# Kernel tuning notes

Hardware: AMD Instinct MI355X
Metric: run time of the kernel (lower is better)

The kernel has to match this reference:

```python
import jax, jax.numpy as jnp
import numpy as np

B, S, D, H, HD = 1, 2048, 1024, 16, 64
GH = 64            # GammaGate hidden dim
FFN_H = int(D * 4 * 2 / 3)
CTX = 512          # omega-rule context window c
LAM = 0.999        # base exponential decay

def _rms(x, w, eps=1e-6):
    return x * jax.lax.rsqrt(jnp.mean(x * x, axis=-1, keepdims=True) + eps) * w

def _rope(q, k):
    hd = q.shape[-1]; s = q.shape[2]
    inv = 1.0 / (10000.0 ** (jnp.arange(0, hd, 2, dtype=jnp.float32) / hd))
    fr = jnp.arange(s, dtype=jnp.float32)[:, None] * inv[None, :]
    cos = jnp.concatenate([jnp.cos(fr), jnp.cos(fr)], -1)
    sin = jnp.concatenate([jnp.sin(fr), jnp.sin(fr)], -1)
    rot = lambda x: jnp.concatenate([-x[..., hd // 2:], x[..., :hd // 2]], -1)
    return q * cos + rot(q) * sin, k * cos + rot(k) * sin

def setup_inputs() -> dict:
    key = jax.random.key(0)
    ks = jax.random.split(key, 10)
    n = lambda i, sh, s=0.02: jax.random.normal(ks[i], sh, jnp.float32) * s
    return dict(
        x=jax.random.normal(ks[0], (B, S, D), jnp.float32),
        norm1_w=jnp.ones((D,), jnp.float32),
        norm2_w=jnp.ones((D,), jnp.float32),
        w_qkv=n(1, (D, 3 * D)),
        q_norm_w=jnp.ones((HD,), jnp.float32),
        k_norm_w=jnp.ones((HD,), jnp.float32),
        gamma_w1=n(2, (D, GH)),
        gamma_w2=n(3, (GH, 1)),
        m_persist=n(4, (H, HD, HD)),
        memory_gate=jnp.array([-3.0], jnp.float32),
        w_o=n(5, (D, D), 0.02 / 2 ** 0.5),
        ffn_w1=n(6, (D, FFN_H)),
        ffn_w3=n(7, (D, FFN_H)),
        ffn_w2=n(8, (FFN_H, D)),
    )

def reference(x, norm1_w, norm2_w, w_qkv, q_norm_w, k_norm_w, gamma_w1, gamma_w2,
              m_persist, memory_gate, w_o, ffn_w1, ffn_w3, ffn_w2):
    b, s, d = x.shape
    h = _rms(x, norm1_w)
    qkv = h @ w_qkv
    q, k, v = jnp.split(qkv, 3, axis=-1)
    rs = lambda t: t.reshape(b, s, H, HD).transpose(0, 2, 1, 3)   # (b,h,s,hd)
    q, k, v = rs(q), rs(k), rs(v)
    q = _rms(q, q_norm_w); k = _rms(k, k_norm_w)                  # qk_norm
    q, k = _rope(q, k)
    # input-dependent gamma gate: Linear->SiLU->Linear->Sigmoid
    gamma = jax.nn.sigmoid(jax.nn.silu(h @ gamma_w1) @ gamma_w2)  # (b,s,1)
    # Omega-rule memory: Q'_t = (M_p q_t + sum_i w_{t,i} k_i (k_i . q_t)) / (1 + sum_i w_{t,i})
    ti = jnp.arange(s)
    delta = ti[:, None] - ti[None, :]
    wmask = (delta >= 0) & (delta < CTX)
    decay = jnp.where(wmask, LAM ** delta.astype(jnp.float32), 0.0)      # (t,i)
    w = decay[None, None] * gamma[:, None, None, :, 0]                   # (b,1,t,i)
    norm = 1.0 + jnp.sum(w, axis=-1)                                     # (b,1,t)
    scores = jnp.einsum('bhtd,bhid->bhti', q, k)
    contrib = jnp.einsum('bhti,bhid->bhtd', w * scores, k)
    persist = jnp.einsum('hde,bhte->bhtd', m_persist, q)
    qp = (persist + contrib) / norm[..., None]
    gate = jax.nn.sigmoid(memory_gate)[0]
    q = (1.0 - gate) * q + gate * qp
    # causal attention
    aw = jnp.einsum('bhtd,bhid->bhti', q, k) * (HD ** -0.5)
    causal = ti[:, None] >= ti[None, :]
    aw = jnp.where(causal[None, None], aw, -jnp.inf)
    aw = jax.nn.softmax(aw, axis=-1)
    ao = jnp.einsum('bhti,bhid->bhtd', aw, v).transpose(0, 2, 1, 3).reshape(b, s, d)
    x = x + ao @ w_o
    h2 = _rms(x, norm2_w)
    x = x + (jax.nn.silu(h2 @ ffn_w1) * (h2 @ ffn_w3)) @ ffn_w2   # SwiGLU
    return x
```

## Files before the change

### kernel.cpp

```cpp
#include <hip/hip_runtime.h>
#include <hip/hip_bf16.h>

#define S_LEN 2048
#define D_DIM 1024
#define H_NUM 16
#define HD_DIM 64
#define GH_DIM 64
#define FFN_H 2730
#define FFNP  2816
#define CTX_W 512
#define L2LAM -0.00144341687f
#define QBLK 64
#define KBLK 64
#define ALDK 76
#define QSCALE 0.1803368801111731f

typedef unsigned short u16;
typedef __attribute__((ext_vector_type(8))) short bf16x8_t;
typedef __attribute__((ext_vector_type(4))) float f32x4_t;

__device__ inline float wave_sum(float v) {
    for (int off = 32; off; off >>= 1) v += __shfl_xor(v, off);
    return v;
}
__device__ inline u16 f2bf(float f) {
    unsigned r;
    asm("v_cvt_pk_bf16_f32 %0, %1, %2" : "=v"(r) : "v"(f), "v"(f));
    return (u16)r;
}
__device__ inline unsigned f2bf2(float lo, float hi) {
    unsigned r;
    asm("v_cvt_pk_bf16_f32 %0, %1, %2" : "=v"(r) : "v"(lo), "v"(hi));
    return r;
}
__device__ inline float bf2f(u16 u) {
    return __uint_as_float(((unsigned int)u) << 16);
}
__device__ inline void gload16(const void* g, void* l) {
    __builtin_amdgcn_global_load_lds(
        (const __attribute__((address_space(1))) void*)g,
        (__attribute__((address_space(3))) void*)l, 16, 0, 0);
}

template<bool GAMMA>
__global__ __launch_bounds__(256) void rmsnorm_gamma_kernel(
    const float* __restrict__ in, const float* __restrict__ w,
    u16* __restrict__ out, const float* __restrict__ w1,
    const float* __restrict__ w2, float* __restrict__ gamma)
{
    __shared__ float hl[D_DIM];
    __shared__ float part[4][GH_DIM];
    __shared__ float wsum[4];
    int row = blockIdx.x;
    int tid = threadIdx.x, lane = tid & 63, wv = tid >> 6;
    const float4* ir = reinterpret_cast<const float4*>(in + (size_t)row * D_DIM);
    float4 v = ir[tid];
    float ss = v.x*v.x + v.y*v.y + v.z*v.z + v.w*v.w;
    ss = wave_sum(ss);
    if (lane == 0) wsum[wv] = ss;
    __syncthreads();
    float tot = wsum[0] + wsum[1] + wsum[2] + wsum[3];
    float scale = rsqrtf(tot / (float)D_DIM + 1e-6f);
    const float4* wr = reinterpret_cast<const float4*>(w);
    float4 wv4 = wr[tid];
    float h0 = v.x * scale * wv4.x, h1 = v.y * scale * wv4.y;
    float h2 = v.z * scale * wv4.z, h3 = v.w * scale * wv4.w;
    uint2 o;
    o.x = f2bf2(h0, h1);
    o.y = f2bf2(h2, h3);
    *reinterpret_cast<uint2*>(out + (size_t)row * D_DIM + tid * 4) = o;
    if (GAMMA) {
        hl[tid*4+0] = h0; hl[tid*4+1] = h1; hl[tid*4+2] = h2; hl[tid*4+3] = h3;
        __syncthreads();
        float acc = 0.f;
        #pragma unroll 8
        for (int k = wv * 256; k < wv * 256 + 256; ++k)
            acc += hl[k] * w1[k * GH_DIM + lane];
        part[wv][lane] = acc;
        __syncthreads();
        if (wv == 0) {
            float t = part[0][lane] + part[1][lane] + part[2][lane] + part[3][lane];
            float z = t / (1.f + __expf(-t));
            float y = z * w2[lane];
            float t2 = wave_sum(y);
            if (lane == 0) gamma[row] = 1.f / (1.f + __expf(-t2));
        }
    }
}

__global__ __launch_bounds__(256) void prep_kernel(
    const float* __restrict__ w_qkv, const float* __restrict__ w_o,
    const float* __restrict__ w1f, const float* __restrict__ w3f,
    const float* __restrict__ w2f, u16* __restrict__ wqT,
    u16* __restrict__ woT, u16* __restrict__ w13T, u16* __restrict__ w2T,
    const float* __restrict__ x, const float* __restrict__ norm1_w,
    u16* __restrict__ h_bf, const float* __restrict__ gw1,
    const float* __restrict__ gw2, float* __restrict__ gamma)
{
    __shared__ float tile[64][65];
    __shared__ float part[4][GH_DIM];
    __shared__ float wsum[4];
    int b = blockIdx.x;
    int tid = threadIdx.x;
    if (b < 3136) {
        const float* src; u16* dst;
        int srcK, srcN, Kp, rowOff, rowMul, nbx;
        if (b < 768)       {           src = w_qkv; dst = wqT;  srcK = 1024; srcN = 3072; Kp = 1024; rowOff = 0; rowMul = 1; nbx = 48; }
        else if (b < 1024) { b -= 768;  src = w_o;  dst = woT;  srcK = 1024; srcN = 1024; Kp = 1024; rowOff = 0; rowMul = 1; nbx = 16; }
        else if (b < 1728) { b -= 1024; src = w1f;  dst = w13T; srcK = 1024; srcN = 2730; Kp = 1024; rowOff = 0; rowMul = 2; nbx = 44; }
        else if (b < 2432) { b -= 1728; src = w3f;  dst = w13T; srcK = 1024; srcN = 2730; Kp = 1024; rowOff = 1; rowMul = 2; nbx = 44; }
        else               { b -= 2432; src = w2f;  dst = w2T;  srcK = 2730; srcN = 1024; Kp = 2816; rowOff = 0; rowMul = 1; nbx = 16; }
        int n0 = (b % nbx) * 64, k0 = (b / nbx) * 64;
        int tx = tid & 15, ty = tid >> 4;
        bool interior = (k0 + 63 < srcK) && (n0 + 63 < srcN);
        #pragma unroll
        for (int p = 0; p < 4; ++p) {
            int kk = p * 16 + ty;
            int r = k0 + kk;
            int cb = n0 + tx * 4;
            float4 v;
            if (interior) {
                v = *(const float4*)(src + (size_t)r * srcN + cb);
            } else {
                v.x = (r < srcK && cb     < srcN) ? src[(size_t)r * srcN + cb]     : 0.f;
                v.y = (r < srcK && cb + 1 < srcN) ? src[(size_t)r * srcN + cb + 1] : 0.f;
                v.z = (r < srcK && cb + 2 < srcN) ? src[(size_t)r * srcN + cb + 2] : 0.f;
                v.w = (r < srcK && cb + 3 < srcN) ? src[(size_t)r * srcN + cb + 3] : 0.f;
            }
            tile[kk][tx*4+0] = v.x; tile[kk][tx*4+1] = v.y;
            tile[kk][tx*4+2] = v.z; tile[kk][tx*4+3] = v.w;
        }
        __syncthreads();
        int wx = tid & 7, wy = tid >> 3;
        #pragma unroll
        for (int p = 0; p < 2; ++p) {
            int nn = p * 32 + wy;
            int ks = wx * 8;
            uint4 o;
            o.x = f2bf2(tile[ks+0][nn], tile[ks+1][nn]);
            o.y = f2bf2(tile[ks+2][nn], tile[ks+3][nn]);
            o.z = f2bf2(tile[ks+4][nn], tile[ks+5][nn]);
            o.w = f2bf2(tile[ks+6][nn], tile[ks+7][nn]);
            *(uint4*)(dst + (size_t)(rowOff + (size_t)(n0 + nn) * rowMul) * Kp + k0 + ks) = o;
        }
    } else {
        int row = b - 3136;
        int lane = tid & 63, wv = tid >> 6;
        float* hl = &tile[0][0];
        const float4* ir = reinterpret_cast<const float4*>(x + (size_t)row * D_DIM);
        float4 v = ir[tid];
        float ss = v.x*v.x + v.y*v.y + v.z*v.z + v.w*v.w;
        ss = wave_sum(ss);
        if (lane == 0) wsum[wv] = ss;
        __syncthreads();
        float tot = wsum[0] + wsum[1] + wsum[2] + wsum[3];
        float scale = rsqrtf(tot / (float)D_DIM + 1e-6f);
        const float4* wr = reinterpret_cast<const float4*>(norm1_w);
        float4 wv4 = wr[tid];
        float h0 = v.x * scale * wv4.x, h1 = v.y * scale * wv4.y;
        float h2 = v.z * scale * wv4.z, h3 = v.w * scale * wv4.w;
        uint2 o;
        o.x = f2bf2(h0, h1);
        o.y = f2bf2(h2, h3);
        *reinterpret_cast<uint2*>(h_bf + (size_t)row * D_DIM + tid * 4) = o;
        hl[tid*4+0] = h0; hl[tid*4+1] = h1; hl[tid*4+2] = h2; hl[tid*4+3] = h3;
        __syncthreads();
        float acc = 0.f;
        #pragma unroll 8
        for (int k = wv * 256; k < wv * 256 + 256; ++k)
            acc += hl[k] * gw1[k * GH_DIM + lane];
        part[wv][lane] = acc;
        __syncthreads();
        if (wv == 0) {
            float t = part[0][lane] + part[1][lane] + part[2][lane] + part[3][lane];
            float z = t / (1.f + __expf(-t));
            float y = z * gw2[lane];
            float t2 = wave_sum(y);
            if (lane == 0) gamma[row] = 1.f / (1.f + __expf(-t2));
        }
    }
}

__global__ __launch_bounds__(256) void split_rope_tr_kernel(
    const u16* __restrict__ qkv, const float* __restrict__ qw,
    const float* __restrict__ kw, float* __restrict__ qhp,
    u16* __restrict__ khp, u16* __restrict__ khT, u16* __restrict__ vhT)
{
    __shared__ u16 tk[64][ALDK];
    __shared__ u16 tv[64][ALDK];
    int tid = threadIdx.x;
    int w = tid >> 6, d = tid & 63;
    int h = blockIdx.y;
    int s0 = blockIdx.x * 64;
    float qwv = qw[d], kwv = kw[d];
    int j = d & 31;
    float inv = expf(-(float)j * (9.2103403719761836f / 32.0f));
    float sgn = (d < 32) ? -1.f : 1.f;
    for (int i = 0; i < 16; ++i) {
        int sl = w * 16 + i;
        int s = s0 + sl;
        size_t base = (size_t)s * (3 * D_DIM) + h * HD_DIM + d;
        float qv = bf2f(qkv[base]);
        float kv = bf2f(qkv[base + D_DIM]);
        u16  vv = qkv[base + 2 * D_DIM];
        float sq = wave_sum(qv * qv);
        float qn = qv * rsqrtf(sq / (float)HD_DIM + 1e-6f) * qwv;
        float sk = wave_sum(kv * kv);
        float kn = kv * rsqrtf(sk / (float)HD_DIM + 1e-6f) * kwv;
        float ang = (float)s * inv;
        float cs = cosf(ang), sn = sinf(ang);
        float qp = __shfl_xor(qn, 32);
        float kp = __shfl_xor(kn, 32);
        float qo = qn * cs + sgn * qp * sn;
        float ko = kn * cs + sgn * kp * sn;
        size_t ob = ((size_t)h * S_LEN + s) * HD_DIM + d;
        u16 kb = f2bf(ko);
        qhp[ob] = qo;
        khp[ob] = kb;
        tk[sl][d] = kb;
        tv[sl][d] = vv;
    }
    __syncthreads();
    int r = tid >> 2, cc = (tid & 3) * 16;
    union { u16 u[16]; bf16x8_t v[2]; } ok, ov;
    #pragma unroll
    for (int e = 0; e < 16; ++e) {
        int ksrc = (e & 3) * 16 + (tid & 3) * 4 + (e >> 2);
        ok.u[e] = tk[ksrc][r]; ov.u[e] = tv[ksrc][r];
    }
    u16* kd = khT + ((size_t)h * HD_DIM + r) * S_LEN + s0 + cc;
    u16* vd = vhT + ((size_t)h * HD_DIM + r) * S_LEN + s0 + cc;
    *(bf16x8_t*)kd       = ok.v[0];
    *(bf16x8_t*)(kd + 8) = ok.v[1];
    *(bf16x8_t*)vd       = ov.v[0];
    *(bf16x8_t*)(vd + 8) = ov.v[1];
}

template<int BM, int MODE>
__global__ __launch_bounds__(256) void gemm_bb_kernel(
    const u16* __restrict__ A, const u16* __restrict__ B,
    u16* __restrict__ Cb, int M, int N, int K)
{
    constexpr int MREP = BM / 32;
    constexpr int ACH  = BM / 32;
    __shared__ u16 As[BM * 64];
    __shared__ u16 Bs[128 * 64];
    int tid = threadIdx.x, lane = tid & 63, wid = tid >> 6;
    int wr = wid >> 1, wc = wid & 1;
    int row0 = blockIdx.y * BM, col0 = blockIdx.x * 128;
    int l8 = lane >> 3, l7 = lane & 7;
    f32x4_t acc[MREP][4];
    #pragma unroll
    for (int i = 0; i < MREP; ++i)
        #pragma unroll
        for (int j = 0; j < 4; ++j) acc[i][j] = (f32x4_t)0.f;

    int fr = lane & 15, fo = (lane >> 4) * 8;
    for (int k0 = 0; k0 < K; k0 += 64) {
        #pragma unroll
        for (int i = 0; i < ACH; ++i) {
            int ch = wid * ACH + i;
            const u16* ga = A + (size_t)(row0 + ch * 8 + l8) * K + k0 + l7 * 8;
            gload16(ga, &As[ch * 512]);
        }
        #pragma unroll
        for (int i = 0; i < 4; ++i) {
            int ch = wid * 4 + i;
            const u16* gb = B + (size_t)(col0 + ch * 8 + l8) * K + k0 + l7 * 8;
            gload16(gb, &Bs[ch * 512]);
        }
        __syncthreads();
        __builtin_amdgcn_s_setprio(1);
        #pragma unroll
        for (int khf = 0; khf < 2; ++khf) {
            bf16x8_t bfrag[4];
            #pragma unroll
            for (int ni = 0; ni < 4; ++ni)
                bfrag[ni] = *(const bf16x8_t*)&Bs[(wc * 64 + ni * 16 + fr) * 64 + khf * 32 + fo];
            #pragma unroll
            for (int mi = 0; mi < MREP; ++mi) {
                bf16x8_t af = *(const bf16x8_t*)&As[(wr * (BM / 2) + mi * 16 + fr) * 64 + khf * 32 + fo];
                #pragma unroll
                for (int ni = 0; ni < 4; ++ni)
                    acc[mi][ni] = __builtin_amdgcn_mfma_f32_16x16x32_bf16(
                        af, bfrag[ni], acc[mi][ni], 0, 0, 0);
            }
        }
        __builtin_amdgcn_s_setprio(0);
        __syncthreads();
    }
    int dr = (lane >> 4) * 4, dc = lane & 15;
    #pragma unroll
    for (int mi = 0; mi < MREP; ++mi) {
        int gr = row0 + wr * (BM / 2) + mi * 16 + dr;
        #pragma unroll
        for (int ni = 0; ni < 4; ++ni) {
            int gc = col0 + wc * 64 + ni * 16 + dc;
            #pragma unroll
            for (int j = 0; j < 4; ++j) {
                float v = acc[mi][ni][j];
                if (MODE == 1) {
                    Cb[(size_t)(gr + j) * N + gc] = f2bf(v);
                } else {
                    float partner = __shfl_xor(v, 1);
                    float a1 = (dc & 1) ? partner : v;
                    float a3 = (dc & 1) ? v : partner;
                    float rr = a1 / (1.f + __expf(-a1)) * a3;
                    if (!(dc & 1))
                        Cb[(size_t)(gr + j) * (N >> 1) + (gc >> 1)] = f2bf(rr);
                }
            }
        }
    }
}

__global__ __launch_bounds__(256) void gemm64_kernel(
    const u16* __restrict__ A, const u16* __restrict__ B,
    const float* __restrict__ res, float* __restrict__ Cf,
    int M, int N, int K)
{
    __shared__ u16 As[64 * 64];
    __shared__ u16 Bs[64 * 64];
    int tid = threadIdx.x, lane = tid & 63, wid = tid >> 6;
    int wr = wid >> 1, wc = wid & 1;
    int row0 = blockIdx.y * 64, col0 = blockIdx.x * 64;
    int l8 = lane >> 3, l7 = lane & 7;
    f32x4_t acc[2][2];
    #pragma unroll
    for (int i = 0; i < 2; ++i)
        #pragma unroll
        for (int j = 0; j < 2; ++j) acc[i][j] = (f32x4_t)0.f;
    int fr = lane & 15, fo = (lane >> 4) * 8;
    for (int k0 = 0; k0 < K; k0 += 64) {
        #pragma unroll
        for (int i = 0; i < 2; ++i) {
            int ch = wid * 2 + i;
            const u16* ga = A + (size_t)(row0 + ch * 8 + l8) * K + k0 + l7 * 8;
            gload16(ga, &As[ch * 512]);
            const u16* gb = B + (size_t)(col0 + ch * 8 + l8) * K + k0 + l7 * 8;
            gload16(gb, &Bs[ch * 512]);
        }
        __syncthreads();
        __builtin_amdgcn_s_setprio(1);
        #pragma unroll
        for (int khf = 0; khf < 2; ++khf) {
            bf16x8_t bfrag[2];
            #pragma unroll
            for (int ni = 0; ni < 2; ++ni)
                bfrag[ni] = *(const bf16x8_t*)&Bs[(wc * 32 + ni * 16 + fr) * 64 + khf * 32 + fo];
            #pragma unroll
            for (int mi = 0; mi < 2; ++mi) {
                bf16x8_t af = *(const bf16x8_t*)&As[(wr * 32 + mi * 16 + fr) * 64 + khf * 32 + fo];
                #pragma unroll
                for (int ni = 0; ni < 2; ++ni)
                    acc[mi][ni] = __builtin_amdgcn_mfma_f32_16x16x32_bf16(
                        af, bfrag[ni], acc[mi][ni], 0, 0, 0);
            }
        }
        __builtin_amdgcn_s_setprio(0);
        __syncthreads();
    }
    int dr = (lane >> 4) * 4, dc = lane & 15;
    #pragma unroll
    for (int mi = 0; mi < 2; ++mi) {
        int gr = row0 + wr * 32 + mi * 16 + dr;
        #pragma unroll
        for (int ni = 0; ni < 2; ++ni) {
            int gc = col0 + wc * 32 + ni * 16 + dc;
            #pragma unroll
            for (int j = 0; j < 4; ++j) {
                size_t off = (size_t)(gr + j) * N + gc;
                Cf[off] = acc[mi][ni][j] + res[off];
            }
        }
    }
}

__global__ __launch_bounds__(256) void fused_omega_attn_kernel(
    const float* __restrict__ qhp, const u16* __restrict__ khp,
    const u16* __restrict__ khT, const u16* __restrict__ vhT,
    const float* __restrict__ gammab, const float* __restrict__ mp,
    const float* __restrict__ mg, u16* __restrict__ ao)
{
    __shared__ u16 Ks[2][KBLK][ALDK];
    __shared__ u16 Xt[2][KBLK][ALDK];
    __shared__ u16 Ps[QBLK][ALDK];
    __shared__ float colfL[CTX_W + KBLK];
    const int tid = threadIdx.x, lane = tid & 63, wq = tid >> 6;
    const int b = blockIdx.x;
    const int hi = (b >> 8) & 1;
    const int h = ((b & 7) << 1) + hi;
    const int s5 = (b >> 3) & 31;
    const int qt = hi ? (31 - s5) : s5;
    const int q0 = qt * QBLK;
    const int fr = lane & 15, g4 = lane >> 4;
    const int fko = g4 * 8;
    const int c = fr, rg = g4;
    const int si = tid >> 2, sdb = (tid & 3) * 16;
    const size_t hS = (size_t)h * S_LEN;
    const size_t hD = (size_t)h * HD_DIM;

    int rowt[4]; float rowf[4];
    #pragma unroll
    for (int j = 0; j < 4; ++j) {
        rowt[j] = q0 + wq * 16 + rg * 4 + j;
        rowf[j] = exp2f((float)(wq * 16 + rg * 4 + j) * L2LAM);
    }
    bf16x8_t qf[2];
    {
        const float* qrow = qhp + (hS + q0 + wq * 16 + fr) * HD_DIM;
        #pragma unroll
        for (int u = 0; u < 2; ++u) {
            float4 a = *(const float4*)(qrow + u * 32 + fko);
            float4 bq = *(const float4*)(qrow + u * 32 + fko + 4);
            bf16x8_t f;
            f[0]=f2bf(a.x); f[1]=f2bf(a.y); f[2]=f2bf(a.z); f[3]=f2bf(a.w);
            f[4]=f2bf(bq.x); f[5]=f2bf(bq.y); f[6]=f2bf(bq.z); f[7]=f2bf(bq.w);
            qf[u] = f;
        }
    }
    f32x4_t accc[4];
    #pragma unroll
    for (int n = 0; n < 4; ++n) accc[n] = (f32x4_t)0.f;
    float wsum[4] = {0.f, 0.f, 0.f, 0.f};
    const int kt0 = (q0 > (CTX_W - 1)) ? (q0 - (CTX_W - 1)) / KBLK : 0;
    const int i0 = kt0 * KBLK;
    const int nwin = (qt + 1) * KBLK - i0;
    for (int idx = tid; idx < nwin; idx += 256) {
        int icol = i0 + idx;
        colfL[idx] = exp2f((float)(q0 - icol) * L2LAM) * gammab[icol];
    }
    {
        const u16* gk = khp + (hS + kt0 * KBLK + si) * HD_DIM + sdb;
        const u16* gx = khT + (hD + si) * S_LEN + kt0 * KBLK + sdb;
        *(bf16x8_t*)&Ks[0][si][sdb]     = *(const bf16x8_t*)gk;
        *(bf16x8_t*)&Ks[0][si][sdb + 8] = *(const bf16x8_t*)(gk + 8);
        *(bf16x8_t*)&Xt[0][si][sdb]     = *(const bf16x8_t*)gx;
        *(bf16x8_t*)&Xt[0][si][sdb + 8] = *(const bf16x8_t*)(gx + 8);
    }
    __syncthreads();
    int cur = 0;
    for (int kt = kt0; kt <= qt; ++kt) {
        const int k0 = kt * KBLK;
        const bool hn = (kt < qt);
        bf16x8_t nk0, nk1, nx0, nx1;
        if (hn) {
            const u16* gk = khp + (hS + k0 + KBLK + si) * HD_DIM + sdb;
            const u16* gx = khT + (hD + si) * S_LEN + k0 + KBLK + sdb;
            nk0 = *(const bf16x8_t*)gk; nk1 = *(const bf16x8_t*)(gk + 8);
            nx0 = *(const bf16x8_t*)gx; nx1 = *(const bf16x8_t*)(gx + 8);
        }
        f32x4_t s[4];
        #pragma unroll
        for (int n = 0; n < 4; ++n) s[n] = (f32x4_t)0.f;
        __builtin_amdgcn_s_setprio(1);
        #pragma unroll
        for (int u = 0; u < 2; ++u)
            #pragma unroll
            for (int n = 0; n < 4; ++n) {
                bf16x8_t kb = *(const bf16x8_t*)&Ks[cur][n * 16 + fr][u * 32 + fko];
                s[n] = __builtin_amdgcn_mfma_f32_16x16x32_bf16(qf[u], kb, s[n], 0, 0, 0);
            }
        __builtin_amdgcn_s_setprio(0);
        const bool boundary = (kt == kt0) || (kt == qt);
        float colf[4];
        #pragma unroll
        for (int n = 0; n < 4; ++n)
            colf[n] = colfL[k0 - i0 + n * 16 + c];
        #pragma unroll
        for (int j = 0; j < 4; ++j) {
            float pv[4];
            #pragma unroll
            for (int n = 0; n < 4; ++n) {
                float w;
                if (boundary) {
                    int delta = rowt[j] - (k0 + n * 16 + c);
                    w = (delta >= 0 && delta < CTX_W) ? rowf[j] * colf[n] : 0.f;
                } else {
                    w = rowf[j] * colf[n];
                }
                wsum[j] += w;
                pv[n] = w * s[n][j];
            }
            uint2 pk;
            pk.x = f2bf2(pv[0], pv[1]);
            pk.y = f2bf2(pv[2], pv[3]);
            *(uint2*)&Ps[wq * 16 + rg * 4 + j][c * 4] = pk;
        }
        __builtin_amdgcn_s_setprio(1);
        #pragma unroll
        for (int u = 0; u < 2; ++u) {
            bf16x8_t pa = *(const bf16x8_t*)&Ps[wq * 16 + fr][u * 32 + fko];
            #pragma unroll
            for (int n = 0; n < 4; ++n) {
                bf16x8_t kb = *(const bf16x8_t*)&Xt[cur][n * 16 + fr][u * 32 + fko];
                accc[n] = __builtin_amdgcn_mfma_f32_16x16x32_bf16(pa, kb, accc[n], 0, 0, 0);
            }
        }
        __builtin_amdgcn_s_setprio(0);
        if (hn) {
            int nxt = cur ^ 1;
            *(bf16x8_t*)&Ks[nxt][si][sdb]     = nk0;
            *(bf16x8_t*)&Ks[nxt][si][sdb + 8] = nk1;
            *(bf16x8_t*)&Xt[nxt][si][sdb]     = nx0;
            *(bf16x8_t*)&Xt[nxt][si][sdb + 8] = nx1;
        }
        __syncthreads();
        cur ^= 1;
    }
    f32x4_t pacc[4];
    #pragma unroll
    for (int n = 0; n < 4; ++n) pacc[n] = (f32x4_t)0.f;
    const float* mph = mp + hD * HD_DIM;
    #pragma unroll
    for (int u = 0; u < 2; ++u)
        #pragma unroll
        for (int n = 0; n < 4; ++n) {
            const float* br = mph + (size_t)(n * 16 + fr) * HD_DIM + u * 32 + fko;
            float4 a = *(const float4*)br;
            float4 bq = *(const float4*)(br + 4);
            bf16x8_t f;
            f[0]=f2bf(a.x); f[1]=f2bf(a.y); f[2]=f2bf(a.z); f[3]=f2bf(a.w);
            f[4]=f2bf(bq.x); f[5]=f2bf(bq.y); f[6]=f2bf(bq.z); f[7]=f2bf(bq.w);
            pacc[n] = __builtin_amdgcn_mfma_f32_16x16x32_bf16(qf[u], f, pacc[n], 0, 0, 0);
        }
    #pragma unroll
    for (int j = 0; j < 4; ++j) {
        wsum[j] += __shfl_xor(wsum[j], 1);
        wsum[j] += __shfl_xor(wsum[j], 2);
        wsum[j] += __shfl_xor(wsum[j], 4);
        wsum[j] += __shfl_xor(wsum[j], 8);
    }
    float gate = 1.f / (1.f + __expf(-mg[0]));
    float keep = 1.f - gate;
    #pragma unroll
    for (int n = 0; n < 4; ++n) {
        #pragma unroll
        for (int j = 0; j < 4; ++j) {
            float qold = qhp[(hS + rowt[j]) * HD_DIM + n * 16 + c];
            float qn = keep * qold + gate * (pacc[n][j] + accc[n][j]) / (1.f + wsum[j]);
            Ps[wq * 16 + rg * 4 + j][n * 16 + c] = f2bf(qn * QSCALE);
        }
    }
    bf16x8_t qf2[2];
    #pragma unroll
    for (int u = 0; u < 2; ++u)
        qf2[u] = *(const bf16x8_t*)&Ps[wq * 16 + fr][u * 32 + fko];

    f32x4_t acco[4];
    #pragma unroll
    for (int n = 0; n < 4; ++n) acco[n] = (f32x4_t)0.f;
    float l_run[4] = {0.f, 0.f, 0.f, 0.f};
    {
        const u16* gk = khp + (hS + si) * HD_DIM + sdb;
        const u16* gv = vhT + (hD + si) * S_LEN + sdb;
        *(bf16x8_t*)&Ks[0][si][sdb]     = *(const bf16x8_t*)gk;
        *(bf16x8_t*)&Ks[0][si][sdb + 8] = *(const bf16x8_t*)(gk + 8);
        *(bf16x8_t*)&Xt[0][si][sdb]     = *(const bf16x8_t*)gv;
        *(bf16x8_t*)&Xt[0][si][sdb + 8] = *(const bf16x8_t*)(gv + 8);
    }
    __syncthreads();
    cur = 0;
    for (int kt = 0; kt <= qt; ++kt) {
        const int k0 = kt * KBLK;
        const bool hn = (kt < qt);
        bf16x8_t nk0, nk1, nv0, nv1;
        if (hn) {
            const u16* gk = khp + (hS + k0 + KBLK + si) * HD_DIM + sdb;
            const u16* gv = vhT + (hD + si) * S_LEN + k0 + KBLK + sdb;
            nk0 = *(const bf16x8_t*)gk; nk1 = *(const bf16x8_t*)(gk + 8);
            nv0 = *(const bf16x8_t*)gv; nv1 = *(const bf16x8_t*)(gv + 8);
        }
        f32x4_t s[4];
        #pragma unroll
        for (int n = 0; n < 4; ++n) s[n] = (f32x4_t)0.f;
        __builtin_amdgcn_s_setprio(1);
        #pragma unroll
        for (int u = 0; u < 2; ++u)
            #pragma unroll
            for (int n = 0; n < 4; ++n) {
                bf16x8_t kb = *(const bf16x8_t*)&Ks[cur][n * 16 + fr][u * 32 + fko];
                s[n] = __builtin_amdgcn_mfma_f32_16x16x32_bf16(qf2[u], kb, s[n], 0, 0, 0);
            }
        __builtin_amdgcn_s_setprio(0);
        if (kt == qt) {
            #pragma unroll
            for (int n = 0; n < 4; ++n) {
                int icol = k0 + n * 16 + c;
                #pragma unroll
                for (int j = 0; j < 4; ++j)
                    if (icol > rowt[j]) s[n][j] = -1e30f;
            }
        }
        #pragma unroll
        for (int j = 0; j < 4; ++j) {
            float p0 = exp2f(s[0][j]);
            float p1 = exp2f(s[1][j]);
            float p2 = exp2f(s[2][j]);
            float p3 = exp2f(s[3][j]);
            l_run[j] += (p0 + p1) + (p2 + p3);
            uint2 pk;
            pk.x = f2bf2(p0, p1);
            pk.y = f2bf2(p2, p3);
            *(uint2*)&Ps[wq * 16 + rg * 4 + j][c * 4] = pk;
        }
        __builtin_amdgcn_s_setprio(1);
        #pragma unroll
        for (int u = 0; u < 2; ++u) {
            bf16x8_t pa = *(const bf16x8_t*)&Ps[wq * 16 + fr][u * 32 + fko];
            #pragma unroll
            for (int n = 0; n < 4; ++n) {
                bf16x8_t vb = *(const bf16x8_t*)&Xt[cur][n * 16 + fr][u * 32 + fko];
                acco[n] = __builtin_amdgcn_mfma_f32_16x16x32_bf16(pa, vb, acco[n], 0, 0, 0);
            }
        }
        __builtin_amdgcn_s_setprio(0);
        if (hn) {
            int nxt = cur ^ 1;
            *(bf16x8_t*)&Ks[nxt][si][sdb]     = nk0;
            *(bf16x8_t*)&Ks[nxt][si][sdb + 8] = nk1;
            *(bf16x8_t*)&Xt[nxt][si][sdb]     = nv0;
            *(bf16x8_t*)&Xt[nxt][si][sdb + 8] = nv1;
        }
        __syncthreads();
        cur ^= 1;
    }
    #pragma unroll
    for (int j = 0; j < 4; ++j) {
        l_run[j] += __shfl_xor(l_run[j], 1);
        l_run[j] += __shfl_xor(l_run[j], 2);
        l_run[j] += __shfl_xor(l_run[j], 4);
        l_run[j] += __shfl_xor(l_run[j], 8);
    }
    #pragma unroll
    for (int n = 0; n < 4; ++n) {
        #pragma unroll
        for (int j = 0; j < 4; ++j) {
            float o = acco[n][j] / l_run[j];
            ao[(size_t)rowt[j] * D_DIM + h * HD_DIM + n * 16 + c] = f2bf(o);
        }
    }
}

extern "C" void kernel_launch(void* const* d_in, const int* in_sizes, int n_in,
                              void* d_out, int out_size, void* d_ws, size_t ws_size,
                              hipStream_t stream) {
    const float* x         = (const float*)d_in[0];
    const float* norm1_w   = (const float*)d_in[1];
    const float* norm2_w   = (const float*)d_in[2];
    const float* w_qkv     = (const float*)d_in[3];
    const float* q_norm_w  = (const float*)d_in[4];
    const float* k_norm_w  = (const float*)d_in[5];
    const float* gamma_w1  = (const float*)d_in[6];
    const float* gamma_w2  = (const float*)d_in[7];
    const float* m_persist = (const float*)d_in[8];
    const float* mem_gate  = (const float*)d_in[9];
    const float* w_o       = (const float*)d_in[10];
    const float* ffn_w1    = (const float*)d_in[11];
    const float* ffn_w3    = (const float*)d_in[12];
    const float* ffn_w2    = (const float*)d_in[13];
    float* out = (float*)d_out;
    char* ws = (char*)d_ws;

    const size_t MB = 1024 * 1024;
    u16*   h_bf   = (u16*)(ws);
    u16*   wqT    = (u16*)(ws + 4 * MB);
    u16*   woT    = (u16*)(ws + 10 * MB);
    u16*   w13T   = (u16*)(ws + 12 * MB);
    u16*   w2T    = (u16*)(ws + 23 * MB);
    u16*   qkv_bf = (u16*)(ws + 29884416);
    u16*   ao_bf  = (u16*)(ws + 38273024);
    float* qh     = (float*)(ws + 42467328);
    u16*   kh     = (u16*)(ws + 50855936);
    u16*   khT_s  = (u16*)(ws + 50855936 + 4 * MB);
    float* gammab = (float*)(ws + 59244544);
    u16*   vhT_s  = (u16*)(ws + 59244544 + 64 * 1024);
    u16*   mid_bf = (u16*)(ws + 29884416);

    hipLaunchKernelGGL(prep_kernel, dim3(3136 + S_LEN), dim3(256), 0, stream,
                       w_qkv, w_o, ffn_w1, ffn_w3, ffn_w2, wqT, woT, w13T, w2T,
                       x, norm1_w, h_bf, gamma_w1, gamma_w2, gammab);

    hipLaunchKernelGGL((gemm_bb_kernel<64, 1>), dim3(24, 32), dim3(256), 0, stream,
                       h_bf, wqT, qkv_bf, S_LEN, 3 * D_DIM, D_DIM);
    hipLaunchKernelGGL(split_rope_tr_kernel, dim3(S_LEN / 64, H_NUM), dim3(256), 0, stream,
                       qkv_bf, q_norm_w, k_norm_w, qh, kh, khT_s, vhT_s);
    hipLaunchKernelGGL(fused_omega_attn_kernel, dim3(512), dim3(256), 0, stream,
                       qh, kh, khT_s, vhT_s, gammab, m_persist, mem_gate, ao_bf);
    hipLaunchKernelGGL(gemm64_kernel, dim3(16, 32), dim3(256), 0, stream,
                       ao_bf, woT, x, out, S_LEN, D_DIM, D_DIM);
    hipLaunchKernelGGL((rmsnorm_gamma_kernel<false>), dim3(S_LEN), dim3(256), 0, stream,
                       out, norm2_w, h_bf, (const float*)nullptr,
                       (const float*)nullptr, (float*)nullptr);
    hipLaunchKernelGGL((gemm_bb_kernel<128, 2>), dim3(44, 16), dim3(256), 0, stream,
                       h_bf, w13T, mid_bf, S_LEN, 2 * FFNP, D_DIM);
    hipLaunchKernelGGL(gemm64_kernel, dim3(16, 32), dim3(256), 0, stream,
                       mid_bf, w2T, out, out, S_LEN, D_DIM, FFNP);
}
```

Before: 221.8 us.

## Split attention columns across two wave groups with 512-thread blocks

The fused omega/attention kernel now runs 8 waves per block instead of 4. Each group of 4 waves computes half of the 64 key/output columns, so per-wave MFMA work and register use are halved. Row sums (wsum, l_run) are combined through a small shared-memory reduction, and the P tile is written cooperatively. This adds an extra __syncthreads per key tile plus reduction barriers in exchange for more waves in flight on each CU.

```diff
diff --git a/kernel.cpp b/kernel.cpp
--- a/kernel.cpp
+++ b/kernel.cpp
@@ -376,7 +376,7 @@
     }
 }
 
-__global__ __launch_bounds__(256) void fused_omega_attn_kernel(
+__global__ __launch_bounds__(512) void fused_omega_attn_kernel(
     const float* __restrict__ qhp, const u16* __restrict__ khp,
     const u16* __restrict__ khT, const u16* __restrict__ vhT,
     const float* __restrict__ gammab, const float* __restrict__ mp,
@@ -386,7 +386,10 @@
     __shared__ u16 Xt[2][KBLK][ALDK];
     __shared__ u16 Ps[QBLK][ALDK];
     __shared__ float colfL[CTX_W + KBLK];
-    const int tid = threadIdx.x, lane = tid & 63, wq = tid >> 6;
+    __shared__ float redS[2][QBLK];
+    const int tid = threadIdx.x, lane = tid & 63, wid = tid >> 6;
+    const int wq = wid & 3;
+    const int nh = wid >> 2;
     const int b = blockIdx.x;
     const int hi = (b >> 8) & 1;
     const int h = ((b & 7) << 1) + hi;
@@ -396,7 +399,7 @@
     const int fr = lane & 15, g4 = lane >> 4;
     const int fko = g4 * 8;
     const int c = fr, rg = g4;
-    const int si = tid >> 2, sdb = (tid & 3) * 16;
+    const int si = tid >> 3, sdb = (tid & 7) * 8;
     const size_t hS = (size_t)h * S_LEN;
     const size_t hD = (size_t)h * HD_DIM;
 
@@ -419,110 +422,108 @@
             qf[u] = f;
         }
     }
-    f32x4_t accc[4];
-    #pragma unroll
-    for (int n = 0; n < 4; ++n) accc[n] = (f32x4_t)0.f;
+    float qold[2][4];
+    #pragma unroll
+    for (int nn = 0; nn < 2; ++nn)
+        #pragma unroll
+        for (int j = 0; j < 4; ++j)
+            qold[nn][j] = qhp[(hS + rowt[j]) * HD_DIM + (nh * 2 + nn) * 16 + c];
+
+    f32x4_t accc[2];
+    accc[0] = (f32x4_t)0.f; accc[1] = (f32x4_t)0.f;
     float wsum[4] = {0.f, 0.f, 0.f, 0.f};
     const int kt0 = (q0 > (CTX_W - 1)) ? (q0 - (CTX_W - 1)) / KBLK : 0;
     const int i0 = kt0 * KBLK;
     const int nwin = (qt + 1) * KBLK - i0;
-    for (int idx = tid; idx < nwin; idx += 256) {
+    for (int idx = tid; idx < nwin; idx += 512) {
         int icol = i0 + idx;
         colfL[idx] = exp2f((float)(q0 - icol) * L2LAM) * gammab[icol];
     }
     {
         const u16* gk = khp + (hS + kt0 * KBLK + si) * HD_DIM + sdb;
         const u16* gx = khT + (hD + si) * S_LEN + kt0 * KBLK + sdb;
-        *(bf16x8_t*)&Ks[0][si][sdb]     = *(const bf16x8_t*)gk;
-        *(bf16x8_t*)&Ks[0][si][sdb + 8] = *(const bf16x8_t*)(gk + 8);
-        *(bf16x8_t*)&Xt[0][si][sdb]     = *(const bf16x8_t*)gx;
-        *(bf16x8_t*)&Xt[0][si][sdb + 8] = *(const bf16x8_t*)(gx + 8);
+        *(bf16x8_t*)&Ks[0][si][sdb] = *(const bf16x8_t*)gk;
+        *(bf16x8_t*)&Xt[0][si][sdb] = *(const bf16x8_t*)gx;
     }
     __syncthreads();
     int cur = 0;
     for (int kt = kt0; kt <= qt; ++kt) {
         const int k0 = kt * KBLK;
         const bool hn = (kt < qt);
-        bf16x8_t nk0, nk1, nx0, nx1;
+        bf16x8_t nk0, nx0;
         if (hn) {
             const u16* gk = khp + (hS + k0 + KBLK + si) * HD_DIM + sdb;
             const u16* gx = khT + (hD + si) * S_LEN + k0 + KBLK + sdb;
-            nk0 = *(const bf16x8_t*)gk; nk1 = *(const bf16x8_t*)(gk + 8);
-            nx0 = *(const bf16x8_t*)gx; nx1 = *(const bf16x8_t*)(gx + 8);
-        }
-        f32x4_t s[4];
-        #pragma unroll
-        for (int n = 0; n < 4; ++n) s[n] = (f32x4_t)0.f;
+            nk0 = *(const bf16x8_t*)gk;
+            nx0 = *(const bf16x8_t*)gx;
+        }
+        f32x4_t s[2];
+        s[0] = (f32x4_t)0.f; s[1] = (f32x4_t)0.f;
         __builtin_amdgcn_s_setprio(1);
         #pragma unroll
         for (int u = 0; u < 2; ++u)
             #pragma unroll
-            for (int n = 0; n < 4; ++n) {
-                bf16x8_t kb = *(const bf16x8_t*)&Ks[cur][n * 16 + fr][u * 32 + fko];
-                s[n] = __builtin_amdgcn_mfma_f32_16x16x32_bf16(qf[u], kb, s[n], 0, 0, 0);
+            for (int nn = 0; nn < 2; ++nn) {
+                bf16x8_t kb = *(const bf16x8_t*)&Ks[cur][(nh * 2 + nn) * 16 + fr][u * 32 + fko];
+                s[nn] = __builtin_amdgcn_mfma_f32_16x16x32_bf16(qf[u], kb, s[nn], 0, 0, 0);
             }
         __builtin_amdgcn_s_setprio(0);
         const bool boundary = (kt == kt0) || (kt == qt);
-        float colf[4];
-        #pragma unroll
-        for (int n = 0; n < 4; ++n)
-            colf[n] = colfL[k0 - i0 + n * 16 + c];
+        float colf[2];
+        #pragma unroll
+        for (int nn = 0; nn < 2; ++nn)
+            colf[nn] = colfL[k0 - i0 + (nh * 2 + nn) * 16 + c];
         #pragma unroll
         for (int j = 0; j < 4; ++j) {
-            float pv[4];
-            #pragma unroll
-            for (int n = 0; n < 4; ++n) {
+            float pv[2];
+            #pragma unroll
+            for (int nn = 0; nn < 2; ++nn) {
                 float w;
                 if (boundary) {
-                    int delta = rowt[j] - (k0 + n * 16 + c);
-                    w = (delta >= 0 && delta < CTX_W) ? rowf[j] * colf[n] : 0.f;
+                    int delta = rowt[j] - (k0 + (nh * 2 + nn) * 16 + c);
+                    w = (delta >= 0 && delta < CTX_W) ? rowf[j] * colf[nn] : 0.f;
                 } else {
-                    w = rowf[j] * colf[n];
+                    w = rowf[j] * colf[nn];
                 }
                 wsum[j] += w;
-                pv[n] = w * s[n][j];
-            }
-            uint2 pk;
-            pk.x = f2bf2(pv[0], pv[1]);
-            pk.y = f2bf2(pv[2], pv[3]);
-            *(uint2*)&Ps[wq * 16 + rg * 4 + j][c * 4] = pk;
-        }
+                pv[nn] = w * s[nn][j];
+            }
+            *(unsigned*)&Ps[wq * 16 + rg * 4 + j][c * 4 + nh * 2] = f2bf2(pv[0], pv[1]);
+        }
+        __syncthreads();
         __builtin_amdgcn_s_setprio(1);
         #pragma unroll
         for (int u = 0; u < 2; ++u) {
             bf16x8_t pa = *(const bf16x8_t*)&Ps[wq * 16 + fr][u * 32 + fko];
             #pragma unroll
-            for (int n = 0; n < 4; ++n) {
-                bf16x8_t kb = *(const bf16x8_t*)&Xt[cur][n * 16 + fr][u * 32 + fko];
-                accc[n] = __builtin_amdgcn_mfma_f32_16x16x32_bf16(pa, kb, accc[n], 0, 0, 0);
+            for (int nn = 0; nn < 2; ++nn) {
+                bf16x8_t kb = *(const bf16x8_t*)&Xt[cur][(nh * 2 + nn) * 16 + fr][u * 32 + fko];
+                accc[nn] = __builtin_amdgcn_mfma_f32_16x16x32_bf16(pa, kb, accc[nn], 0, 0, 0);
             }
         }
         __builtin_amdgcn_s_setprio(0);
         if (hn) {
             int nxt = cur ^ 1;
-            *(bf16x8_t*)&Ks[nxt][si][sdb]     = nk0;
-            *(bf16x8_t*)&Ks[nxt][si][sdb + 8] = nk1;
-            *(bf16x8_t*)&Xt[nxt][si][sdb]     = nx0;
-            *(bf16x8_t*)&Xt[nxt][si][sdb + 8] = nx1;
+            *(bf16x8_t*)&Ks[nxt][si][sdb] = nk0;
+            *(bf16x8_t*)&Xt[nxt][si][sdb] = nx0;
         }
         __syncthreads();
         cur ^= 1;
     }
-    f32x4_t pacc[4];
-    #pragma unroll
-    for (int n = 0; n < 4; ++n) pacc[n] = (f32x4_t)0.f;
+    f32x4_t pacc[2];
+    pacc[0] = (f32x4_t)0.f; pacc[1] = (f32x4_t)0.f;
     const float* mph = mp + hD * HD_DIM;
     #pragma unroll
     for (int u = 0; u < 2; ++u)
         #pragma unroll
-        for (int n = 0; n < 4; ++n) {
-            const float* br = mph + (size_t)(n * 16 + fr) * HD_DIM + u * 32 + fko;
+        for (int nn = 0; nn < 2; ++nn) {
+            const float* br = mph + (size_t)((nh * 2 + nn) * 16 + fr) * HD_DIM + u * 32 + fko;
             float4 a = *(const float4*)br;
             float4 bq = *(const float4*)(br + 4);
             bf16x8_t f;
             f[0]=f2bf(a.x); f[1]=f2bf(a.y); f[2]=f2bf(a.z); f[3]=f2bf(a.w);
             f[4]=f2bf(bq.x); f[5]=f2bf(bq.y); f[6]=f2bf(bq.z); f[7]=f2bf(bq.w);
-            pacc[n] = __builtin_amdgcn_mfma_f32_16x16x32_bf16(qf[u], f, pacc[n], 0, 0, 0);
+            pacc[nn] = __builtin_amdgcn_mfma_f32_16x16x32_bf16(qf[u], f, pacc[nn], 0, 0, 0);
         }
     #pragma unroll
     for (int j = 0; j < 4; ++j) {
@@ -531,96 +532,96 @@
         wsum[j] += __shfl_xor(wsum[j], 4);
         wsum[j] += __shfl_xor(wsum[j], 8);
     }
+    if (fr == 0) {
+        #pragma unroll
+        for (int j = 0; j < 4; ++j)
+            redS[nh][wq * 16 + rg * 4 + j] = wsum[j];
+    }
+    __syncthreads();
+    float wtot[4];
+    #pragma unroll
+    for (int j = 0; j < 4; ++j)
+        wtot[j] = redS[0][wq * 16 + rg * 4 + j] + redS[1][wq * 16 + rg * 4 + j];
     float gate = 1.f / (1.f + __expf(-mg[0]));
     float keep = 1.f - gate;
     #pragma unroll
-    for (int n = 0; n < 4; ++n) {
+    for (int nn = 0; nn < 2; ++nn) {
         #pragma unroll
         for (int j = 0; j < 4; ++j) {
-            float qold = qhp[(hS + rowt[j]) * HD_DIM + n * 16 + c];
-            float qn = keep * qold + gate * (pacc[n][j] + accc[n][j]) / (1.f + wsum[j]);
-            Ps[wq * 16 + rg * 4 + j][n * 16 + c] = f2bf(qn * QSCALE);
-        }
-    }
+            float qn = keep * qold[nn][j] + gate * (pacc[nn][j] + accc[nn][j]) / (1.f + wtot[j]);
+            Ps[wq * 16 + rg * 4 + j][(nh * 2 + nn) * 16 + c] = f2bf(qn * QSCALE);
+        }
+    }
+    __syncthreads();
     bf16x8_t qf2[2];
     #pragma unroll
     for (int u = 0; u < 2; ++u)
         qf2[u] = *(const bf16x8_t*)&Ps[wq * 16 + fr][u * 32 + fko];
 
-    f32x4_t acco[4];
-    #pragma unroll
-    for (int n = 0; n < 4; ++n) acco[n] = (f32x4_t)0.f;
+    f32x4_t acco[2];
+    acco[0] = (f32x4_t)0.f; acco[1] = (f32x4_t)0.f;
     float l_run[4] = {0.f, 0.f, 0.f, 0.f};
     {
         const u16* gk = khp + (hS + si) * HD_DIM + sdb;
         const u16* gv = vhT + (hD + si) * S_LEN + sdb;
-        *(bf16x8_t*)&Ks[0][si][sdb]     = *(const bf16x8_t*)gk;
-        *(bf16x8_t*)&Ks[0][si][sdb + 8] = *(const bf16x8_t*)(gk + 8);
-        *(bf16x8_t*)&Xt[0][si][sdb]     = *(const bf16x8_t*)gv;
-        *(bf16x8_t*)&Xt[0][si][sdb + 8] = *(const bf16x8_t*)(gv + 8);
+        *(bf16x8_t*)&Ks[0][si][sdb] = *(const bf16x8_t*)gk;
+        *(bf16x8_t*)&Xt[0][si][sdb] = *(const bf16x8_t*)gv;
     }
     __syncthreads();
     cur = 0;
     for (int kt = 0; kt <= qt; ++kt) {
         const int k0 = kt * KBLK;
         const bool hn = (kt < qt);
-        bf16x8_t nk0, nk1, nv0, nv1;
+        bf16x8_t nk0, nv0;
         if (hn) {
             const u16* gk = khp + (hS + k0 + KBLK + si) * HD_DIM + sdb;
             const u16* gv = vhT + (hD + si) * S_LEN + k0 + KBLK + sdb;
-            nk0 = *(const bf16x8_t*)gk; nk1 = *(const bf16x8_t*)(gk + 8);
-            nv0 = *(const bf16x8_t*)gv; nv1 = *(const bf16x8_t*)(gv + 8);
-        }
-        f32x4_t s[4];
-        #pragma unroll
-        for (int n = 0; n < 4; ++n) s[n] = (f32x4_t)0.f;
+            nk0 = *(const bf16x8_t*)gk;
+            nv0 = *(const bf16x8_t*)gv;
+        }
+        f32x4_t s[2];
+        s[0] = (f32x4_t)0.f; s[1] = (f32x4_t)0.f;
         __builtin_amdgcn_s_setprio(1);
         #pragma unroll
         for (int u = 0; u < 2; ++u)
             #pragma unroll
-            for (int n = 0; n < 4; ++n) {
-                bf16x8_t kb = *(const bf16x8_t*)&Ks[cur][n * 16 + fr][u * 32 + fko];
-                s[n] = __builtin_amdgcn_mfma_f32_16x16x32_bf16(qf2[u], kb, s[n], 0, 0, 0);
+            for (int nn = 0; nn < 2; ++nn) {
+                bf16x8_t kb = *(const bf16x8_t*)&Ks[cur][(nh * 2 + nn) * 16 + fr][u * 32 + fko];
+                s[nn] = __builtin_amdgcn_mfma_f32_16x16x32_bf16(qf2[u], kb, s[nn], 0, 0, 0);
             }
         __builtin_amdgcn_s_setprio(0);
         if (kt == qt) {
             #pragma unroll
-            for (int n = 0; n < 4; ++n) {
-                int icol = k0 + n * 16 + c;
+            for (int nn = 0; nn < 2; ++nn) {
+                int icol = k0 + (nh * 2 + nn) * 16 + c;
                 #pragma unroll
                 for (int j = 0; j < 4; ++j)
-                    if (icol > rowt[j]) s[n][j] = -1e30f;
+                    if (icol > rowt[j]) s[nn][j] = -1e30f;
             }
         }
         #pragma unroll
         for (int j = 0; j < 4; ++j) {
             float p0 = exp2f(s[0][j]);
             float p1 = exp2f(s[1][j]);
-            float p2 = exp2f(s[2][j]);
-            float p3 = exp2f(s[3][j]);
-            l_run[j] += (p0 + p1) + (p2 + p3);
-            uint2 pk;
-            pk.x = f2bf2(p0, p1);
-            pk.y = f2bf2(p2, p3);
-            *(uint2*)&Ps[wq * 16 + rg * 4 + j][c * 4] = pk;
-        }
+            l_run[j] += p0 + p1;
+            *(unsigned*)&Ps[wq * 16 + rg * 4 + j][c * 4 + nh * 2] = f2bf2(p0, p1);
+        }
+        __syncthreads();
         __builtin_amdgcn_s_setprio(1);
         #pragma unroll
         for (int u = 0; u < 2; ++u) {
             bf16x8_t pa = *(const bf16x8_t*)&Ps[wq * 16 + fr][u * 32 + fko];
             #pragma unroll
-            for (int n = 0; n < 4; ++n) {
-                bf16x8_t vb = *(const bf16x8_t*)&Xt[cur][n * 16 + fr][u * 32 + fko];
-                acco[n] = __builtin_amdgcn_mfma_f32_16x16x32_bf16(pa, vb, acco[n], 0, 0, 0);
+            for (int nn = 0; nn < 2; ++nn) {
+                bf16x8_t vb = *(const bf16x8_t*)&Xt[cur][(nh * 2 + nn) * 16 + fr][u * 32 + fko];
+                acco[nn] = __builtin_amdgcn_mfma_f32_16x16x32_bf16(pa, vb, acco[nn], 0, 0, 0);
             }
         }
         __builtin_amdgcn_s_setprio(0);
         if (hn) {
             int nxt = cur ^ 1;
-            *(bf16x8_t*)&Ks[nxt][si][sdb]     = nk0;
-            *(bf16x8_t*)&Ks[nxt][si][sdb + 8] = nk1;
-            *(bf16x8_t*)&Xt[nxt][si][sdb]     = nv0;
-            *(bf16x8_t*)&Xt[nxt][si][sdb + 8] = nv1;
+            *(bf16x8_t*)&Ks[nxt][si][sdb] = nk0;
+            *(bf16x8_t*)&Xt[nxt][si][sdb] = nv0;
         }
         __syncthreads();
         cur ^= 1;
@@ -632,12 +633,21 @@
         l_run[j] += __shfl_xor(l_run[j], 4);
         l_run[j] += __shfl_xor(l_run[j], 8);
     }
-    #pragma unroll
-    for (int n = 0; n < 4; ++n) {
+    if (fr == 0) {
+        #pragma unroll
+        for (int j = 0; j < 4; ++j)
+            redS[nh][wq * 16 + rg * 4 + j] = l_run[j];
+    }
+    __syncthreads();
+    #pragma unroll
+    for (int j = 0; j < 4; ++j)
+        l_run[j] = redS[0][wq * 16 + rg * 4 + j] + redS[1][wq * 16 + rg * 4 + j];
+    #pragma unroll
+    for (int nn = 0; nn < 2; ++nn) {
         #pragma unroll
         for (int j = 0; j < 4; ++j) {
-            float o = acco[n][j] / l_run[j];
-            ao[(size_t)rowt[j] * D_DIM + h * HD_DIM + n * 16 + c] = f2bf(o);
+            float o = acco[nn][j] / l_run[j];
+            ao[(size_t)rowt[j] * D_DIM + h * HD_DIM + (nh * 2 + nn) * 16 + c] = f2bf(o);
         }
     }
 }
@@ -685,7 +695,7 @@
                        h_bf, wqT, qkv_bf, S_LEN, 3 * D_DIM, D_DIM);
     hipLaunchKernelGGL(split_rope_tr_kernel, dim3(S_LEN / 64, H_NUM), dim3(256), 0, stream,
                        qkv_bf, q_norm_w, k_norm_w, qh, kh, khT_s, vhT_s);
-    hipLaunchKernelGGL(fused_omega_attn_kernel, dim3(512), dim3(256), 0, stream,
+    hipLaunchKernelGGL(fused_omega_attn_kernel, dim3(512), dim3(512), 0, stream,
                        qh, kh, khT_s, vhT_s, gammab, m_persist, mem_gate, ao_bf);
     hipLaunchKernelGGL(gemm64_kernel, dim3(16, 32), dim3(256), 0, stream,
                        ao_bf, woT, x, out, S_LEN, D_DIM, D_DIM);
```

After: 217.9 us. Within noise of the previous version (-1.8%).
